# Kernel tuning notes

Hardware: AMD Instinct MI355X
Metric: run time of the kernel (lower is better)

The kernel has to match this reference:

```python
import jax, jax.numpy as jnp
import numpy as np

# LSNNParameters defaults (norse)
TAU_SYN_INV = 200.0     # 1/tau_syn
TAU_MEM_INV = 100.0     # 1/tau_mem
TAU_ADAPT_INV = 1.0 / 800.0  # 1/tau_adapt
V_LEAK = 0.0
V_TH = 1.0
V_RESET = 0.0
BETA = 1.8
DT = 0.001

B, IN_F, OUT_F = 8192, 512, 1024


def setup_inputs() -> dict:
    key = jax.random.key(0)
    k0, k1, k2, k3, k4, k5, k6 = jax.random.split(key, 7)
    input_spikes = (jax.random.uniform(k0, (B, IN_F)) < 0.2).astype(jnp.float32)
    z = (jax.random.uniform(k1, (B, OUT_F)) < 0.2).astype(jnp.float32)
    v = jax.random.normal(k2, (B, OUT_F)) * 0.5
    i = jax.random.normal(k3, (B, OUT_F)) * 0.5
    b = jax.random.uniform(k4, (B, OUT_F))
    input_weights = jax.random.normal(k5, (OUT_F, IN_F)) / np.sqrt(IN_F)
    recurrent_weights = jax.random.normal(k6, (OUT_F, OUT_F))
    return {
        "input_spikes": input_spikes,
        "z": z,
        "v": v,
        "i": i,
        "b": b,
        "input_weights": input_weights,
        "recurrent_weights": recurrent_weights,
    }


def reference(input_spikes, z, v, i, b, input_weights, recurrent_weights):
    # One euler step of the LSNN cell (norse lsnn_step).
    # voltage update: dv = dt * tau_mem_inv * ((v_leak - v) + i)
    v_decayed = v + DT * TAU_MEM_INV * ((V_LEAK - v) + i)
    # current decay: di = -dt * tau_syn_inv * i
    i_decayed = i + DT * (-TAU_SYN_INV) * i
    # adaptive threshold relaxes toward v_th
    b_decayed = b + DT * TAU_ADAPT_INV * (V_TH - b)
    # spike condition (heaviside jump)
    z_new = (v_decayed - b_decayed > 0).astype(v.dtype)
    # reset
    v_new = (1.0 - z_new) * v_decayed + z_new * V_RESET
    # current jumps from input + recurrent synapses (x @ W^T, torch linear)
    i_new = (
        i_decayed
        + jnp.einsum("bi,oi->bo", input_spikes, input_weights)
        + jnp.einsum("bo,no->bn", z, recurrent_weights)
    )
    # threshold adaptation
    b_new = b_decayed + z_new * TAU_ADAPT_INV * BETA
    # stack (z, v, i, b) new state -> [4, B, OUT_F]
    return jnp.stack([z_new, v_new, i_new, b_new])
```

## Files before the change

kernel.cpp:

```cpp
#include <hip/hip_runtime.h>

#define B_ROWS 8192
#define IN_F 512
#define OUT_F 1024
#define K_TOT 1536

#define BM 64
#define BN 64
#define BK 64
#define NITER (K_TOT / BK)

#define A4_COUNT (B_ROWS * (K_TOT / 4))
#define W4_COUNT (OUT_F  * (K_TOT / 4))
#define CAST_BLOCKS ((A4_COUNT + W4_COUNT) / 1024)
#define GEMM_BLOCKS ((B_ROWS / BM) * (OUT_F / BN))
#define P_BLOCKS ((B_ROWS * OUT_F / 4) / 1024)
#define FUSED_BLOCKS (GEMM_BLOCKS + P_BLOCKS)

typedef short bfrag __attribute__((ext_vector_type(8)));
typedef float f4    __attribute__((ext_vector_type(4)));

__device__ __forceinline__ unsigned int pack2bf(float a, float b) {
    unsigned int ua = __float_as_uint(a);
    unsigned int ub = __float_as_uint(b);
    ua = (ua + 0x7fffu + ((ua >> 16) & 1u)) >> 16;
    ub = (ub + 0x7fffu + ((ub >> 16) & 1u)) & 0xffff0000u;
    return ua | ub;
}

__global__ __launch_bounds__(256) void precast_aw(
    const float* __restrict__ spikes, const float* __restrict__ zin,
    const float* __restrict__ Wi,     const float* __restrict__ Wr,
    unsigned short* __restrict__ Abf, unsigned short* __restrict__ Wbf)
{
    const int base = blockIdx.x * 1024 + threadIdx.x;
    const float4* src[4];
    #pragma unroll
    for (int k = 0; k < 4; ++k) {
        const int idx = base + k * 256;
        if (idx < A4_COUNT) {
            const int row = idx / 384, c4 = idx - row * 384;
            src[k] = (const float4*)((c4 < 128)
                         ? spikes + (size_t)row * IN_F + c4 * 4
                         : zin    + (size_t)row * OUT_F + (c4 - 128) * 4);
        } else {
            const int w = idx - A4_COUNT;
            const int row = w / 384, c4 = w - row * 384;
            src[k] = (const float4*)((c4 < 128)
                         ? Wi + (size_t)row * IN_F + c4 * 4
                         : Wr + (size_t)row * OUT_F + (c4 - 128) * 4);
        }
    }
    float4 val[4];
    #pragma unroll
    for (int k = 0; k < 4; ++k) val[k] = *src[k];
    #pragma unroll
    for (int k = 0; k < 4; ++k) {
        const int idx = base + k * 256;
        unsigned short* dst = (idx < A4_COUNT)
                                  ? Abf + (size_t)idx * 4
                                  : Wbf + (size_t)(idx - A4_COUNT) * 4;
        uint2 pk = { pack2bf(val[k].x, val[k].y), pack2bf(val[k].z, val[k].w) };
        *(uint2*)dst = pk;
    }
}

__device__ __forceinline__ void pointwise_block(
    int pb, int tid,
    const float* __restrict__ vin, const float* __restrict__ iin,
    const float* __restrict__ bin, float* __restrict__ out)
{
    const size_t PL = (size_t)B_ROWS * OUT_F;
    const int base = pb * 1024 + tid;
    const f4* v4 = (const f4*)vin;
    const f4* i4 = (const f4*)iin;
    const f4* b4 = (const f4*)bin;
    f4 vv[4], ii[4], bb[4];
    #pragma unroll
    for (int k = 0; k < 4; ++k) vv[k] = v4[base + k * 256];
    #pragma unroll
    for (int k = 0; k < 4; ++k) ii[k] = i4[base + k * 256];
    #pragma unroll
    for (int k = 0; k < 4; ++k) bb[k] = b4[base + k * 256];
    #pragma unroll
    for (int k = 0; k < 4; ++k) {
        f4 z, vn, bn;
        #pragma unroll
        for (int c = 0; c < 4; ++c) {
            const float v_dec = vv[k][c] + 0.1f * (ii[k][c] - vv[k][c]);
            const float b_dec = bb[k][c] + 1.25e-06f * (1.0f - bb[k][c]);
            const float zz = (v_dec - b_dec > 0.0f) ? 1.0f : 0.0f;
            z[c]  = zz;
            vn[c] = (1.0f - zz) * v_dec;
            bn[c] = b_dec + zz * 0.00225f;
        }
        const int j = base + k * 256;
        __builtin_nontemporal_store(z,  (f4*)out + j);
        __builtin_nontemporal_store(vn, (f4*)(out + PL) + j);
        __builtin_nontemporal_store(bn, (f4*)(out + 3 * PL) + j);
    }
}

__global__ __launch_bounds__(256, 4) void lsnn_gemm(
    const unsigned short* __restrict__ Abf,
    const unsigned short* __restrict__ Wbf,
    const float* __restrict__ vin,
    const float* __restrict__ iin,
    const float* __restrict__ bin,
    float* __restrict__ out)
{
    __shared__ unsigned short As[2][BM * BK];
    __shared__ unsigned short Ws[2][BN * BK];

    const int tid = threadIdx.x;
    const int octet = blockIdx.x >> 3;
    const int sub   = blockIdx.x & 7;
    const int id    = (octet >> 1) * 8 + sub;

    if (octet & 1) {
        pointwise_block(id, tid, vin, iin, bin, out);
        return;
    }

    const int n0 = (id & 15) * BN;
    const int m0 = (id >> 4) * BM;

    const int lane = tid & 63;
    const int wave = tid >> 6;
    const int wm = (wave >> 1) * 32;
    const int wn = (wave & 1) * 32;
    const int lr = lane & 15;
    const int lq = lane >> 4;

    f4 acc[2][2];
    #pragma unroll
    for (int a = 0; a < 2; ++a)
        #pragma unroll
        for (int b = 0; b < 2; ++b)
            acc[a][b] = (f4)0.0f;

    const unsigned short* Ab = Abf + (size_t)m0 * K_TOT;
    const unsigned short* Wb = Wbf + (size_t)n0 * K_TOT;

    int rr[2], cc_[2], jj[2];
    #pragma unroll
    for (int p = 0; p < 2; ++p) {
        const int q = p * 256 + wave * 64 + lane;
        rr[p] = q >> 3;
        cc_[p] = (q & 7) ^ (rr[p] & 7);
        jj[p] = p * 256 + wave * 64;
    }

    auto stage = [&](int buf, int kt) {
        #pragma unroll
        for (int p = 0; p < 2; ++p)
            __builtin_amdgcn_global_load_lds(
                (const __attribute__((address_space(1))) void*)(Ab + (size_t)rr[p] * K_TOT + kt + cc_[p] * 8),
                (__attribute__((address_space(3))) void*)(&As[buf][jj[p] * 8]),
                16, 0, 0);
        #pragma unroll
        for (int p = 0; p < 2; ++p)
            __builtin_amdgcn_global_load_lds(
                (const __attribute__((address_space(1))) void*)(Wb + (size_t)rr[p] * K_TOT + kt + cc_[p] * 8),
                (__attribute__((address_space(3))) void*)(&Ws[buf][jj[p] * 8]),
                16, 0, 0);
    };

    stage(0, 0);
    __syncthreads();

    int cur = 0;
    for (int it = 0; it < NITER; ++it) {
        if (it + 1 < NITER) stage(cur ^ 1, (it + 1) * BK);

        #pragma unroll
        for (int ks = 0; ks < 2; ++ks) {
            const int cc = ks * 4 + lq;
            bfrag af[2], wf[2];
            #pragma unroll
            for (int t = 0; t < 2; ++t) {
                const int row = wm + t * 16 + lr;
                af[t] = *(const bfrag*)&As[cur][row * BK + ((cc ^ (row & 7)) << 3)];
            }
            #pragma unroll
            for (int t = 0; t < 2; ++t) {
                const int row = wn + t * 16 + lr;
                wf[t] = *(const bfrag*)&Ws[cur][row * BK + ((cc ^ (row & 7)) << 3)];
            }
            #pragma unroll
            for (int tm = 0; tm < 2; ++tm)
                #pragma unroll
                for (int tn = 0; tn < 2; ++tn)
                    acc[tm][tn] = __builtin_amdgcn_mfma_f32_16x16x32_bf16(
                        af[tm], wf[tn], acc[tm][tn], 0, 0, 0);
        }

        __syncthreads();
        cur ^= 1;
    }

    const size_t PL2 = 2 * (size_t)B_ROWS * OUT_F;
    #pragma unroll
    for (int tm = 0; tm < 2; ++tm) {
        #pragma unroll
        for (int tn = 0; tn < 2; ++tn) {
            #pragma unroll
            for (int r = 0; r < 4; ++r) {
                const int gm = m0 + wm + tm * 16 + lq * 4 + r;
                const int gn = n0 + wn + tn * 16 + lr;
                const size_t idx = (size_t)gm * OUT_F + gn;
                const float i = iin[idx];
                __builtin_nontemporal_store((i - 0.2f * i) + acc[tm][tn][r],
                                            &out[PL2 + idx]);
            }
        }
    }
}

extern "C" void kernel_launch(void* const* d_in, const int* in_sizes, int n_in,
                              void* d_out, int out_size, void* d_ws, size_t ws_size,
                              hipStream_t stream) {
    const float* spikes = (const float*)d_in[0];
    const float* z      = (const float*)d_in[1];
    const float* v      = (const float*)d_in[2];
    const float* i      = (const float*)d_in[3];
    const float* b      = (const float*)d_in[4];
    const float* Wi     = (const float*)d_in[5];
    const float* Wr     = (const float*)d_in[6];
    float* out = (float*)d_out;

    unsigned short* Abf = (unsigned short*)d_ws;
    unsigned short* Wbf = Abf + (size_t)B_ROWS * K_TOT;

    precast_aw<<<CAST_BLOCKS, 256, 0, stream>>>(spikes, z, Wi, Wr, Abf, Wbf);

    lsnn_gemm<<<FUSED_BLOCKS, 256, 0, stream>>>(Abf, Wbf, v, i, b, out);
}
```

Baseline: 314.5 us.

## Fold pointwise state update into GEMM blocks instead of separate interleaved blocks

Each GEMM block now also handles one 1024-float4 chunk of the pointwise v/b/z update. It issues the v, i, b loads before the K loop and writes the results after it. This halves the grid and lets the pointwise load latency overlap the MFMA main loop. In exchange, 48 extra registers stay live across the GEMM loop, which may reduce occupancy or cause spills.

Measured after the change: 297.2 us. 5.5% less time.

```diff
diff --git a/kernel.cpp b/kernel.cpp
--- a/kernel.cpp
+++ b/kernel.cpp
@@ -14,8 +14,6 @@
 #define W4_COUNT (OUT_F  * (K_TOT / 4))
 #define CAST_BLOCKS ((A4_COUNT + W4_COUNT) / 1024)
 #define GEMM_BLOCKS ((B_ROWS / BM) * (OUT_F / BN))
-#define P_BLOCKS ((B_ROWS * OUT_F / 4) / 1024)
-#define FUSED_BLOCKS (GEMM_BLOCKS + P_BLOCKS)
 
 typedef short bfrag __attribute__((ext_vector_type(8)));
 typedef float f4    __attribute__((ext_vector_type(4)));
@@ -65,42 +63,6 @@
     }
 }
 
-__device__ __forceinline__ void pointwise_block(
-    int pb, int tid,
-    const float* __restrict__ vin, const float* __restrict__ iin,
-    const float* __restrict__ bin, float* __restrict__ out)
-{
-    const size_t PL = (size_t)B_ROWS * OUT_F;
-    const int base = pb * 1024 + tid;
-    const f4* v4 = (const f4*)vin;
-    const f4* i4 = (const f4*)iin;
-    const f4* b4 = (const f4*)bin;
-    f4 vv[4], ii[4], bb[4];
-    #pragma unroll
-    for (int k = 0; k < 4; ++k) vv[k] = v4[base + k * 256];
-    #pragma unroll
-    for (int k = 0; k < 4; ++k) ii[k] = i4[base + k * 256];
-    #pragma unroll
-    for (int k = 0; k < 4; ++k) bb[k] = b4[base + k * 256];
-    #pragma unroll
-    for (int k = 0; k < 4; ++k) {
-        f4 z, vn, bn;
-        #pragma unroll
-        for (int c = 0; c < 4; ++c) {
-            const float v_dec = vv[k][c] + 0.1f * (ii[k][c] - vv[k][c]);
-            const float b_dec = bb[k][c] + 1.25e-06f * (1.0f - bb[k][c]);
-            const float zz = (v_dec - b_dec > 0.0f) ? 1.0f : 0.0f;
-            z[c]  = zz;
-            vn[c] = (1.0f - zz) * v_dec;
-            bn[c] = b_dec + zz * 0.00225f;
-        }
-        const int j = base + k * 256;
-        __builtin_nontemporal_store(z,  (f4*)out + j);
-        __builtin_nontemporal_store(vn, (f4*)(out + PL) + j);
-        __builtin_nontemporal_store(bn, (f4*)(out + 3 * PL) + j);
-    }
-}
-
 __global__ __launch_bounds__(256, 4) void lsnn_gemm(
     const unsigned short* __restrict__ Abf,
     const unsigned short* __restrict__ Wbf,
@@ -113,17 +75,22 @@
     __shared__ unsigned short Ws[2][BN * BK];
 
     const int tid = threadIdx.x;
-    const int octet = blockIdx.x >> 3;
-    const int sub   = blockIdx.x & 7;
-    const int id    = (octet >> 1) * 8 + sub;
-
-    if (octet & 1) {
-        pointwise_block(id, tid, vin, iin, bin, out);
-        return;
-    }
-
-    const int n0 = (id & 15) * BN;
-    const int m0 = (id >> 4) * BM;
+    const int bid = blockIdx.x;
+
+    const int pw = bid * 1024 + tid;
+    const f4* v4 = (const f4*)vin;
+    const f4* i4 = (const f4*)iin;
+    const f4* b4 = (const f4*)bin;
+    f4 vv[4], ii[4], bb[4];
+    #pragma unroll
+    for (int k = 0; k < 4; ++k) vv[k] = v4[pw + k * 256];
+    #pragma unroll
+    for (int k = 0; k < 4; ++k) ii[k] = i4[pw + k * 256];
+    #pragma unroll
+    for (int k = 0; k < 4; ++k) bb[k] = b4[pw + k * 256];
+
+    const int n0 = (bid & 15) * BN;
+    const int m0 = (bid >> 4) * BM;
 
     const int lane = tid & 63;
     const int wave = tid >> 6;
@@ -199,7 +166,26 @@
         cur ^= 1;
     }
 
-    const size_t PL2 = 2 * (size_t)B_ROWS * OUT_F;
+    const size_t PL = (size_t)B_ROWS * OUT_F;
+    #pragma unroll
+    for (int k = 0; k < 4; ++k) {
+        f4 z, vn, bn;
+        #pragma unroll
+        for (int c = 0; c < 4; ++c) {
+            const float v_dec = vv[k][c] + 0.1f * (ii[k][c] - vv[k][c]);
+            const float b_dec = bb[k][c] + 1.25e-06f * (1.0f - bb[k][c]);
+            const float zz = (v_dec - b_dec > 0.0f) ? 1.0f : 0.0f;
+            z[c]  = zz;
+            vn[c] = (1.0f - zz) * v_dec;
+            bn[c] = b_dec + zz * 0.00225f;
+        }
+        const int j = pw + k * 256;
+        __builtin_nontemporal_store(z,  (f4*)out + j);
+        __builtin_nontemporal_store(vn, (f4*)(out + PL) + j);
+        __builtin_nontemporal_store(bn, (f4*)(out + 3 * PL) + j);
+    }
+
+    const size_t PL2 = 2 * PL;
     #pragma unroll
     for (int tm = 0; tm < 2; ++tm) {
         #pragma unroll
@@ -234,5 +220,5 @@
 
     precast_aw<<<CAST_BLOCKS, 256, 0, stream>>>(spikes, z, Wi, Wr, Abf, Wbf);
 
-    lsnn_gemm<<<FUSED_BLOCKS, 256, 0, stream>>>(Abf, Wbf, v, i, b, out);
-}
+    lsnn_gemm<<<GEMM_BLOCKS, 256, 0, stream>>>(Abf, Wbf, v, i, b, out);
+}
```
